# Optimization experiments

Hardware: AMD Instinct MI355X
Metric: run time of the kernel (lower is better)

Reference implementation:

```python
import jax, jax.numpy as jnp
import numpy as np

N_NODES = 50000
N_EDGES = 800000
OUT_DIM = 394
BN_EPS = 1e-5


def setup_inputs() -> dict:
    key = jax.random.key(0)
    ks = jax.random.split(key, 10)
    x = jax.random.normal(ks[0], (N_NODES, 2), dtype=jnp.float32)
    edge_index = jax.random.randint(ks[1], (2, N_EDGES), 0, N_NODES, dtype=jnp.int64)
    W_gcn = jax.random.normal(ks[2], (OUT_DIM, 2), dtype=jnp.float32) * 0.5
    b_gcn = jax.random.normal(ks[3], (OUT_DIM,), dtype=jnp.float32) * 0.1
    bn_gamma = jax.random.normal(ks[4], (OUT_DIM,), dtype=jnp.float32) * 0.1 + 1.0
    bn_beta = jax.random.normal(ks[5], (OUT_DIM,), dtype=jnp.float32) * 0.1
    bn_mean = jax.random.normal(ks[6], (OUT_DIM,), dtype=jnp.float32) * 0.1
    bn_var = jax.random.uniform(ks[7], (OUT_DIM,), dtype=jnp.float32, minval=0.5, maxval=1.5)
    fc_w = jax.random.normal(ks[8], (OUT_DIM, OUT_DIM), dtype=jnp.float32) * (1.0 / np.sqrt(OUT_DIM))
    fc_b = jax.random.normal(ks[9], (OUT_DIM,), dtype=jnp.float32) * 0.1
    return {"x": x, "edge_index": edge_index, "W_gcn": W_gcn, "b_gcn": b_gcn,
            "bn_gamma": bn_gamma, "bn_beta": bn_beta, "bn_mean": bn_mean,
            "bn_var": bn_var, "fc_w": fc_w, "fc_b": fc_b}


def reference(x, edge_index, W_gcn, b_gcn, bn_gamma, bn_beta, bn_mean, bn_var, fc_w, fc_b):
    n = x.shape[0]
    loop = jnp.arange(n, dtype=edge_index.dtype)
    # PyG GCNConv: add self-loops, symmetric deg^{-1/2} normalization
    src = jnp.concatenate([edge_index[0], loop])  # [E+N] message sources
    dst = jnp.concatenate([edge_index[1], loop])  # [E+N] message targets
    deg = jax.ops.segment_sum(jnp.ones_like(dst, dtype=x.dtype), dst, num_segments=n)
    dinv = jnp.where(deg > 0, jax.lax.rsqrt(deg), 0.0)
    norm = dinv[src] * dinv[dst]  # [E+N]
    xl = x @ W_gcn.T  # [N, 394] linear transform before aggregation
    msgs = xl[src] * norm[:, None]  # [E+N, 394] gathered + normalized messages
    agg = jax.ops.segment_sum(msgs, dst, num_segments=n) + b_gcn  # scatter-add
    h = jax.nn.relu(agg)
    # BatchNorm1d in eval mode (running stats)
    h = (h - bn_mean) * jax.lax.rsqrt(bn_var + BN_EPS) * bn_gamma + bn_beta
    # dropout is a no-op in eval mode
    z = h @ fc_w.T + fc_b
    return (jax.nn.log_softmax(z, axis=1), z)
```

## Files before the change

kernel.cpp:

```cpp
#include <hip/hip_runtime.h>
#include <math.h>

#define DIM 394
#define KP  416
#define NT  13
#define NP  448
#define BN_EPS 1e-5f
#define MAXD 96

typedef __bf16 bf16x8 __attribute__((ext_vector_type(8)));
typedef float  f32x4  __attribute__((ext_vector_type(4)));

__device__ inline bool edges_are_int32(const int* ei) {
    int l = threadIdx.x & 63;
    unsigned long long b = __ballot(ei[2 * l + 1] != 0);
    return b != 0ULL;
}


__global__ void prep_kernel(const float* __restrict__ Wg, const float* __restrict__ bg,
                            const float* __restrict__ gamma, const float* __restrict__ beta,
                            const float* __restrict__ mean, const float* __restrict__ var,
                            const float* __restrict__ fcw,
                            uint4* __restrict__ zbase, float4* __restrict__ Pk,
                            float* __restrict__ Ok, bf16x8* __restrict__ Bp,
                            int z4, int zb) {
    int b = blockIdx.x, t = threadIdx.x;
    if (b < zb) {
        int i = b * 256 + t;
        if (i < z4) zbase[i] = make_uint4(0u, 0u, 0u, 0u);
    } else if (b < zb + 2) {
        int k = (b - zb) * 256 + t;
        if (k < KP) {
            float4 p = make_float4(0.f, 0.f, 0.f, 0.f);
            float o = 0.f;
            if (k < DIM) {
                p.x = Wg[2 * k];
                p.y = Wg[2 * k + 1];
                p.z = bg[k];
                float s = gamma[k] * rsqrtf(var[k] + BN_EPS);
                p.w = s;
                o = beta[k] - s * mean[k];
            }
            Pk[k] = p;
            Ok[k] = o;
        }
    } else {
        int idx = (b - zb - 2) * 256 + t;
        if (idx < NT * 4 * NP) {
            int col = idx % NP;
            int r   = idx / NP;
            int k0  = r * 8;
            bf16x8 v;
            #pragma unroll
            for (int q = 0; q < 8; ++q) {
                int k = k0 + q;
                float f = (col < DIM && k < DIM) ? fcw[col * DIM + k] : 0.0f;
                v[q] = (__bf16)f;
            }
            Bp[idx] = v;
        }
    }
}

__global__ void place_kernel(const int* __restrict__ ei,
                             unsigned* __restrict__ degc,
                             unsigned* __restrict__ payload,
                             unsigned* __restrict__ ocnt,
                             uint2* __restrict__ olist, int e) {
    bool is32 = edges_are_int32(ei);
    int i0 = (blockIdx.x * blockDim.x + threadIdx.x) * 4;
    if (i0 >= e) return;
    int s[4], d[4];
    int cnt = 4;
    if (i0 + 4 <= e) {
        if (is32) {
            int4 sv = *reinterpret_cast<const int4*>(&ei[i0]);
            int4 dv = *reinterpret_cast<const int4*>(&ei[e + i0]);
            s[0] = sv.x; s[1] = sv.y; s[2] = sv.z; s[3] = sv.w;
            d[0] = dv.x; d[1] = dv.y; d[2] = dv.z; d[3] = dv.w;
        } else {
            int4 a = *reinterpret_cast<const int4*>(&ei[2 * i0]);
            int4 b = *reinterpret_cast<const int4*>(&ei[2 * i0 + 4]);
            int4 c = *reinterpret_cast<const int4*>(&ei[2 * (e + i0)]);
            int4 dd = *reinterpret_cast<const int4*>(&ei[2 * (e + i0) + 4]);
            s[0] = a.x; s[1] = a.z; s[2] = b.x; s[3] = b.z;
            d[0] = c.x; d[1] = c.z; d[2] = dd.x; d[3] = dd.z;
        }
    } else {
        cnt = e - i0;
        for (int j = 0; j < cnt; ++j) {
            s[j] = is32 ? ei[i0 + j]     : ei[2 * (i0 + j)];
            d[j] = is32 ? ei[e + i0 + j] : ei[2 * (e + i0 + j)];
        }
    }
    #pragma unroll
    for (int j = 0; j < 4; ++j) {
        if (j >= cnt) break;
        unsigned t = atomicAdd(&degc[d[j]], 1u);
        if (t < MAXD) {
            payload[(size_t)d[j] * MAXD + t] = (unsigned)s[j];
        } else {
            unsigned o = atomicAdd(ocnt, 1u);
            olist[o] = make_uint2((unsigned)s[j], (unsigned)d[j]);
        }
    }
}

__global__ void cleanup_kernel(const uint2* __restrict__ olist,
                               const unsigned* __restrict__ ocnt,
                               const unsigned* __restrict__ degc,
                               const float2* __restrict__ x2,
                               float* __restrict__ yover) {
    unsigned cnt = *ocnt;
    int gstride = gridDim.x * blockDim.x;
    for (unsigned i = blockIdx.x * blockDim.x + threadIdx.x; i < cnt; i += gstride) {
        uint2 sd = olist[i];
        float ds = rsqrtf(1.0f + (float)degc[sd.x]);
        float2 xv = x2[sd.x];
        atomicAdd(&yover[2 * sd.y],     ds * xv.x);
        atomicAdd(&yover[2 * sd.y + 1], ds * xv.y);
    }
}

__global__ __launch_bounds__(256, 2)
void gemm_fused(const float2* __restrict__ x2, const unsigned* __restrict__ degc,
                const unsigned* __restrict__ payload, const float* __restrict__ yover,
                const float4* __restrict__ Pk, const float* __restrict__ Ok,
                const bf16x8* __restrict__ Bp, const float* __restrict__ fcb,
                float* __restrict__ outp, float* __restrict__ z, int n) {
    __shared__ bf16x8 As[2][256];
    __shared__ float2 red[64][4];

    int tid = threadIdx.x;
    int wv  = tid >> 6;
    int l   = tid & 63;
    int cg_ = tid & 15;
    int kg  = l >> 4;
    int row0 = blockIdx.x * 64;
    int gi = row0 + l;

    float y0 = 0.f, y1 = 0.f;
    {
        float2 psum = make_float2(0.f, 0.f);
        float dinv_i = 0.f;
        float2 xi = make_float2(0.f, 0.f);
        if (gi < n) {
            unsigned dg = degc[gi];
            dinv_i = rsqrtf(1.0f + (float)dg);
            xi = x2[gi];
            unsigned m = dg < MAXD ? dg : MAXD;
            const unsigned* pl = payload + (size_t)gi * MAXD;
            for (unsigned t = wv; t < m; t += 4) {
                unsigned s = pl[t];
                float2 xv = x2[s];
                float ds = rsqrtf(1.0f + (float)degc[s]);
                psum.x = fmaf(ds, xv.x, psum.x);
                psum.y = fmaf(ds, xv.y, psum.y);
            }
            if (wv == 0) {
                psum.x += yover[2 * gi];
                psum.y += yover[2 * gi + 1];
            }
        }
        red[l][wv] = psum;
        __syncthreads();
        if (gi < n) {
            float sx = red[l][0].x + red[l][1].x + red[l][2].x + red[l][3].x;
            float sy = red[l][0].y + red[l][1].y + red[l][2].y + red[l][3].y;
            y0 = dinv_i * (sx + dinv_i * xi.x);
            y1 = dinv_i * (sy + dinv_i * xi.y);
        }
    }

    f32x4 acc[4][7];
    #pragma unroll
    for (int a = 0; a < 4; ++a)
        #pragma unroll
        for (int b = 0; b < 7; ++b)
            acc[a][b] = (f32x4){0.f, 0.f, 0.f, 0.f};

    auto stageA = [&](int ks, int buf) {
        int kb = ks * 32 + wv * 8;
        bf16x8 hv;
        #pragma unroll
        for (int q = 0; q < 8; ++q) {
            float4 p = Pk[kb + q];
            float t = fmaf(y0, p.x, fmaf(y1, p.y, p.z));
            t = fmaxf(t, 0.f);
            hv[q] = (__bf16)fmaf(p.w, t, Ok[kb + q]);
        }
        As[buf][wv * 64 + l] = hv;
    };

    const bf16x8* bptr = Bp + (kg * 448 + wv * 112 + cg_);

    bf16x8 Bcur[7], Bnxt[7];
    #pragma unroll
    for (int c = 0; c < 7; ++c) Bcur[c] = bptr[c * 16];
    stageA(0, 0);
    __syncthreads();

    int buf = 0;
    for (int ks = 0; ks < NT; ++ks) {
        if (ks < NT - 1) {
            const bf16x8* bn = bptr + (size_t)(ks + 1) * (4 * 448);
            #pragma unroll
            for (int c = 0; c < 7; ++c) Bnxt[c] = bn[c * 16];
            stageA(ks + 1, buf ^ 1);
        }
        bf16x8 af[4];
        #pragma unroll
        for (int rt = 0; rt < 4; ++rt)
            af[rt] = As[buf][kg * 64 + rt * 16 + cg_];
        #pragma unroll
        for (int ct = 0; ct < 7; ++ct)
            #pragma unroll
            for (int rt = 0; rt < 4; ++rt)
                acc[rt][ct] = __builtin_amdgcn_mfma_f32_16x16x32_bf16(
                                  af[rt], Bcur[ct], acc[rt][ct], 0, 0, 0);
        __syncthreads();
        #pragma unroll
        for (int c = 0; c < 7; ++c) Bcur[c] = Bnxt[c];
        buf ^= 1;
    }

    float* redm = (float*)&As[0][0];
    float* reds = redm + 256;

    int colb = wv * 112;
    float bias[7];
    bool  cv[7];
    #pragma unroll
    for (int ct = 0; ct < 7; ++ct) {
        int c = colb + ct * 16 + cg_;
        cv[ct] = (c < DIM);
        bias[ct] = cv[ct] ? fcb[c] : 0.f;
    }
    #pragma unroll
    for (int rt = 0; rt < 4; ++rt)
        #pragma unroll
        for (int ct = 0; ct < 7; ++ct)
            acc[rt][ct] = acc[rt][ct] + bias[ct];

    f32x4 mx[4];
    #pragma unroll
    for (int rt = 0; rt < 4; ++rt) {
        f32x4 m = (f32x4){-1e30f, -1e30f, -1e30f, -1e30f};
        #pragma unroll
        for (int ct = 0; ct < 7; ++ct) {
            if (!cv[ct]) continue;
            #pragma unroll
            for (int j = 0; j < 4; ++j) m[j] = fmaxf(m[j], acc[rt][ct][j]);
        }
        #pragma unroll
        for (int msk = 1; msk < 16; msk <<= 1)
            #pragma unroll
            for (int j = 0; j < 4; ++j)
                m[j] = fmaxf(m[j], __shfl_xor(m[j], msk));
        mx[rt] = m;
    }
    if (cg_ == 0) {
        #pragma unroll
        for (int rt = 0; rt < 4; ++rt)
            #pragma unroll
            for (int j = 0; j < 4; ++j)
                redm[(rt * 16 + kg * 4 + j) * 4 + wv] = mx[rt][j];
    }
    __syncthreads();
    f32x4 gm[4];
    #pragma unroll
    for (int rt = 0; rt < 4; ++rt)
        #pragma unroll
        for (int j = 0; j < 4; ++j) {
            int r = (rt * 16 + kg * 4 + j) * 4;
            gm[rt][j] = fmaxf(fmaxf(redm[r], redm[r + 1]),
                              fmaxf(redm[r + 2], redm[r + 3]));
        }

    f32x4 sm[4];
    #pragma unroll
    for (int rt = 0; rt < 4; ++rt) {
        f32x4 s = (f32x4){0.f, 0.f, 0.f, 0.f};
        #pragma unroll
        for (int ct = 0; ct < 7; ++ct) {
            if (!cv[ct]) continue;
            #pragma unroll
            for (int j = 0; j < 4; ++j)
                s[j] += __expf(acc[rt][ct][j] - gm[rt][j]);
        }
        #pragma unroll
        for (int msk = 1; msk < 16; msk <<= 1)
            #pragma unroll
            for (int j = 0; j < 4; ++j)
                s[j] += __shfl_xor(s[j], msk);
        sm[rt] = s;
    }
    if (cg_ == 0) {
        #pragma unroll
        for (int rt = 0; rt < 4; ++rt)
            #pragma unroll
            for (int j = 0; j < 4; ++j)
                reds[(rt * 16 + kg * 4 + j) * 4 + wv] = sm[rt][j];
    }
    __syncthreads();
    f32x4 lse[4];
    #pragma unroll
    for (int rt = 0; rt < 4; ++rt)
        #pragma unroll
        for (int j = 0; j < 4; ++j) {
            int r = (rt * 16 + kg * 4 + j) * 4;
            float t = reds[r] + reds[r + 1] + reds[r + 2] + reds[r + 3];
            lse[rt][j] = gm[rt][j] + __logf(t);
        }

    #pragma unroll
    for (int rt = 0; rt < 4; ++rt)
        #pragma unroll
        for (int j = 0; j < 4; ++j) {
            int grow = row0 + rt * 16 + kg * 4 + j;
            if (grow >= n) continue;
            size_t base = (size_t)grow * DIM;
            float L = lse[rt][j];
            #pragma unroll
            for (int ct = 0; ct < 7; ++ct) {
                if (!cv[ct]) continue;
                int c = colb + ct * 16 + cg_;
                float zv = acc[rt][ct][j];
                z[base + c]    = zv;
                outp[base + c] = zv - L;
            }
        }
}

extern "C" void kernel_launch(void* const* d_in, const int* in_sizes, int n_in,
                              void* d_out, int out_size, void* d_ws, size_t ws_size,
                              hipStream_t stream) {
    int n = in_sizes[0] / 2;
    int e = in_sizes[1] / 2;

    const float2* x2   = (const float2*)d_in[0];
    const int*   ei    = (const int*)d_in[1];
    const float* Wg    = (const float*)d_in[2];
    const float* bg    = (const float*)d_in[3];
    const float* gamma = (const float*)d_in[4];
    const float* beta  = (const float*)d_in[5];
    const float* mean  = (const float*)d_in[6];
    const float* var   = (const float*)d_in[7];
    const float* fcw   = (const float*)d_in[8];
    const float* fcb   = (const float*)d_in[9];

    float* out = (float*)d_out;
    float* z   = out + (size_t)n * DIM;

    char* wsb = (char*)d_ws;
    unsigned* degc  = (unsigned*)wsb;
    float*    yover = (float*)(degc + n);
    unsigned* ocnt  = (unsigned*)(yover + 2 * (size_t)n);
    uint2*    olist = (uint2*)(ocnt + 4);
    unsigned* payload = (unsigned*)(olist + e);
    size_t off = (size_t)(3 * n + 4) * 4 + (size_t)e * 8 + (size_t)n * MAXD * 4;
    off = (off + 255) & ~(size_t)255;
    bf16x8* Bp = (bf16x8*)(wsb + off);
    off += (size_t)NT * 4 * NP * 16;
    float4* Pk = (float4*)(wsb + off);
    off += (size_t)KP * 16;
    float* Ok  = (float*)(wsb + off);

    int zwords = 3 * n + 4;
    int z4 = (zwords + 3) / 4;
    int zb = (z4 + 255) / 256;
    int prep_blocks = zb + 2 + (NT * 4 * NP + 255) / 256;
    int eb4 = (e / 4 + 255) / 256 + 1;

    prep_kernel<<<prep_blocks, 256, 0, stream>>>(Wg, bg, gamma, beta, mean, var,
                                                 fcw, (uint4*)degc, Pk, Ok, Bp,
                                                 z4, zb);
    place_kernel<<<eb4, 256, 0, stream>>>(ei, degc, payload, ocnt, olist, e);
    cleanup_kernel<<<64, 256, 0, stream>>>(olist, ocnt, degc, x2, yover);

    int gm = (n + 63) / 64;
    gemm_fused<<<gm, 256, 0, stream>>>(x2, degc, payload, yover, Pk, Ok, Bp,
                                       fcb, out, z, n);
}
```

Before: 129.0 us.

## Split neighbor gather into its own kernel and halve GEMM row tile

```diff
diff --git a/kernel.cpp b/kernel.cpp
--- a/kernel.cpp
+++ b/kernel.cpp
@@ -6,9 +6,10 @@
 #define NT  13
 #define NP  448
 #define BN_EPS 1e-5f
-#define MAXD 96
+#define MAXD 32
 
 typedef __bf16 bf16x8 __attribute__((ext_vector_type(8)));
+typedef __bf16 bf16x4 __attribute__((ext_vector_type(4)));
 typedef float  f32x4  __attribute__((ext_vector_type(4)));
 
 __device__ inline bool edges_are_int32(const int* ei) {
@@ -123,74 +124,79 @@
     }
 }
 
-__global__ __launch_bounds__(256, 2)
-void gemm_fused(const float2* __restrict__ x2, const unsigned* __restrict__ degc,
-                const unsigned* __restrict__ payload, const float* __restrict__ yover,
+__global__ __launch_bounds__(256)
+void gather_kernel(const float2* __restrict__ x2, const unsigned* __restrict__ degc,
+                   const unsigned* __restrict__ payload, const float* __restrict__ yover,
+                   float2* __restrict__ y2, int n) {
+    int tid = blockIdx.x * blockDim.x + threadIdx.x;
+    int gi = tid >> 2;
+    int ln = tid & 3;
+    if (gi >= n) return;
+    unsigned dg = degc[gi];
+    unsigned m = dg < MAXD ? dg : MAXD;
+    const unsigned* pl = payload + (size_t)gi * MAXD;
+    float sx = 0.f, sy = 0.f;
+    for (unsigned t = ln; t < m; t += 4) {
+        unsigned s = pl[t];
+        float ds = rsqrtf(1.0f + (float)degc[s]);
+        float2 xv = x2[s];
+        sx = fmaf(ds, xv.x, sx);
+        sy = fmaf(ds, xv.y, sy);
+    }
+    sx += __shfl_xor(sx, 1); sy += __shfl_xor(sy, 1);
+    sx += __shfl_xor(sx, 2); sy += __shfl_xor(sy, 2);
+    if (ln == 0) {
+        float di = rsqrtf(1.0f + (float)dg);
+        float2 xi = x2[gi];
+        sx += yover[2 * gi];
+        sy += yover[2 * gi + 1];
+        y2[gi] = make_float2(di * (sx + di * xi.x), di * (sy + di * xi.y));
+    }
+}
+
+__global__ __launch_bounds__(256, 3)
+void gemm_fused(const float2* __restrict__ y2,
                 const float4* __restrict__ Pk, const float* __restrict__ Ok,
                 const bf16x8* __restrict__ Bp, const float* __restrict__ fcb,
                 float* __restrict__ outp, float* __restrict__ z, int n) {
-    __shared__ bf16x8 As[2][256];
-    __shared__ float2 red[64][4];
+    __shared__ bf16x4 As4[2][256];
 
     int tid = threadIdx.x;
     int wv  = tid >> 6;
     int l   = tid & 63;
     int cg_ = tid & 15;
     int kg  = l >> 4;
-    int row0 = blockIdx.x * 64;
-    int gi = row0 + l;
-
+    int row0 = blockIdx.x * 32;
+
+    int srow = tid & 31;
+    int skc  = (tid >> 5) & 3;
+    int shalf = tid >> 7;
+    int gi = row0 + srow;
     float y0 = 0.f, y1 = 0.f;
-    {
-        float2 psum = make_float2(0.f, 0.f);
-        float dinv_i = 0.f;
-        float2 xi = make_float2(0.f, 0.f);
-        if (gi < n) {
-            unsigned dg = degc[gi];
-            dinv_i = rsqrtf(1.0f + (float)dg);
-            xi = x2[gi];
-            unsigned m = dg < MAXD ? dg : MAXD;
-            const unsigned* pl = payload + (size_t)gi * MAXD;
-            for (unsigned t = wv; t < m; t += 4) {
-                unsigned s = pl[t];
-                float2 xv = x2[s];
-                float ds = rsqrtf(1.0f + (float)degc[s]);
-                psum.x = fmaf(ds, xv.x, psum.x);
-                psum.y = fmaf(ds, xv.y, psum.y);
-            }
-            if (wv == 0) {
-                psum.x += yover[2 * gi];
-                psum.y += yover[2 * gi + 1];
-            }
-        }
-        red[l][wv] = psum;
-        __syncthreads();
-        if (gi < n) {
-            float sx = red[l][0].x + red[l][1].x + red[l][2].x + red[l][3].x;
-            float sy = red[l][0].y + red[l][1].y + red[l][2].y + red[l][3].y;
-            y0 = dinv_i * (sx + dinv_i * xi.x);
-            y1 = dinv_i * (sy + dinv_i * xi.y);
-        }
-    }
-
-    f32x4 acc[4][7];
-    #pragma unroll
-    for (int a = 0; a < 4; ++a)
+    if (gi < n) {
+        float2 yv = y2[gi];
+        y0 = yv.x;
+        y1 = yv.y;
+    }
+
+    f32x4 acc[2][7];
+    #pragma unroll
+    for (int a = 0; a < 2; ++a)
         #pragma unroll
         for (int b = 0; b < 7; ++b)
             acc[a][b] = (f32x4){0.f, 0.f, 0.f, 0.f};
 
     auto stageA = [&](int ks, int buf) {
-        int kb = ks * 32 + wv * 8;
-        bf16x8 hv;
-        #pragma unroll
-        for (int q = 0; q < 8; ++q) {
+        int kb = ks * 32 + skc * 8 + shalf * 4;
+        bf16x4 hv;
+        #pragma unroll
+        for (int q = 0; q < 4; ++q) {
             float4 p = Pk[kb + q];
             float t = fmaf(y0, p.x, fmaf(y1, p.y, p.z));
             t = fmaxf(t, 0.f);
             hv[q] = (__bf16)fmaf(p.w, t, Ok[kb + q]);
         }
-        As[buf][wv * 64 + l] = hv;
+        As4[buf][(skc * 32 + srow) * 2 + shalf] = hv;
     };
 
     const bf16x8* bptr = Bp + (kg * 448 + wv * 112 + cg_);
@@ -209,14 +215,15 @@
             for (int c = 0; c < 7; ++c) Bnxt[c] = bn[c * 16];
             stageA(ks + 1, buf ^ 1);
         }
-        bf16x8 af[4];
-        #pragma unroll
-        for (int rt = 0; rt < 4; ++rt)
-            af[rt] = As[buf][kg * 64 + rt * 16 + cg_];
+        const bf16x8* As8 = (const bf16x8*)&As4[buf][0];
+        bf16x8 af[2];
+        #pragma unroll
+        for (int rt = 0; rt < 2; ++rt)
+            af[rt] = As8[kg * 32 + rt * 16 + cg_];
         #pragma unroll
         for (int ct = 0; ct < 7; ++ct)
             #pragma unroll
-            for (int rt = 0; rt < 4; ++rt)
+            for (int rt = 0; rt < 2; ++rt)
                 acc[rt][ct] = __builtin_amdgcn_mfma_f32_16x16x32_bf16(
                                   af[rt], Bcur[ct], acc[rt][ct], 0, 0, 0);
         __syncthreads();
@@ -225,8 +232,8 @@
         buf ^= 1;
     }
 
-    float* redm = (float*)&As[0][0];
-    float* reds = redm + 256;
+    float* redm = (float*)&As4[0][0];
+    float* reds = redm + 128;
 
     int colb = wv * 112;
     float bias[7];
@@ -238,14 +245,14 @@
         bias[ct] = cv[ct] ? fcb[c] : 0.f;
     }
     #pragma unroll
-    for (int rt = 0; rt < 4; ++rt)
+    for (int rt = 0; rt < 2; ++rt)
         #pragma unroll
         for (int ct = 0; ct < 7; ++ct)
             acc[rt][ct] = acc[rt][ct] + bias[ct];
 
-    f32x4 mx[4];
-    #pragma unroll
-    for (int rt = 0; rt < 4; ++rt) {
+    f32x4 mx[2];
+    #pragma unroll
+    for (int rt = 0; rt < 2; ++rt) {
         f32x4 m = (f32x4){-1e30f, -1e30f, -1e30f, -1e30f};
         #pragma unroll
         for (int ct = 0; ct < 7; ++ct) {
@@ -262,15 +269,15 @@
     }
     if (cg_ == 0) {
         #pragma unroll
-        for (int rt = 0; rt < 4; ++rt)
+        for (int rt = 0; rt < 2; ++rt)
             #pragma unroll
             for (int j = 0; j < 4; ++j)
                 redm[(rt * 16 + kg * 4 + j) * 4 + wv] = mx[rt][j];
     }
     __syncthreads();
-    f32x4 gm[4];
-    #pragma unroll
-    for (int rt = 0; rt < 4; ++rt)
+    f32x4 gm[2];
+    #pragma unroll
+    for (int rt = 0; rt < 2; ++rt)
         #pragma unroll
         for (int j = 0; j < 4; ++j) {
             int r = (rt * 16 + kg * 4 + j) * 4;
@@ -278,9 +285,9 @@
                               fmaxf(redm[r + 2], redm[r + 3]));
         }
 
-    f32x4 sm[4];
-    #pragma unroll
-    for (int rt = 0; rt < 4; ++rt) {
+    f32x4 sm[2];
+    #pragma unroll
+    for (int rt = 0; rt < 2; ++rt) {
         f32x4 s = (f32x4){0.f, 0.f, 0.f, 0.f};
         #pragma unroll
         for (int ct = 0; ct < 7; ++ct) {
@@ -298,15 +305,15 @@
     }
     if (cg_ == 0) {
         #pragma unroll
-        for (int rt = 0; rt < 4; ++rt)
+        for (int rt = 0; rt < 2; ++rt)
             #pragma unroll
             for (int j = 0; j < 4; ++j)
                 reds[(rt * 16 + kg * 4 + j) * 4 + wv] = sm[rt][j];
     }
     __syncthreads();
-    f32x4 lse[4];
-    #pragma unroll
-    for (int rt = 0; rt < 4; ++rt)
+    f32x4 lse[2];
+    #pragma unroll
+    for (int rt = 0; rt < 2; ++rt)
         #pragma unroll
         for (int j = 0; j < 4; ++j) {
             int r = (rt * 16 + kg * 4 + j) * 4;
@@ -315,7 +322,7 @@
         }
 
     #pragma unroll
-    for (int rt = 0; rt < 4; ++rt)
+    for (int rt = 0; rt < 2; ++rt)
         #pragma unroll
         for (int j = 0; j < 4; ++j) {
             int grow = row0 + rt * 16 + kg * 4 + j;
@@ -357,9 +364,12 @@
     unsigned* degc  = (unsigned*)wsb;
     float*    yover = (float*)(degc + n);
     unsigned* ocnt  = (unsigned*)(yover + 2 * (size_t)n);
-    uint2*    olist = (uint2*)(ocnt + 4);
-    unsigned* payload = (unsigned*)(olist + e);
-    size_t off = (size_t)(3 * n + 4) * 4 + (size_t)e * 8 + (size_t)n * MAXD * 4;
+    float2*   y2    = (float2*)(ocnt + 4);
+    uint2*    olist = (uint2*)(y2 + n);
+    size_t off = (size_t)(5 * n + 4) * 4 + (size_t)e * 8;
+    off = (off + 255) & ~(size_t)255;
+    unsigned* payload = (unsigned*)(wsb + off);
+    off += (size_t)n * MAXD * 4;
     off = (off + 255) & ~(size_t)255;
     bf16x8* Bp = (bf16x8*)(wsb + off);
     off += (size_t)NT * 4 * NP * 16;
@@ -378,8 +388,9 @@
                                                  z4, zb);
     place_kernel<<<eb4, 256, 0, stream>>>(ei, degc, payload, ocnt, olist, e);
     cleanup_kernel<<<64, 256, 0, stream>>>(olist, ocnt, degc, x2, yover);
-
-    int gm = (n + 63) / 64;
-    gemm_fused<<<gm, 256, 0, stream>>>(x2, degc, payload, yover, Pk, Ok, Bp,
-                                       fcb, out, z, n);
-}
+    gather_kernel<<<(4 * n + 255) / 256, 256, 0, stream>>>(x2, degc, payload,
+                                                           yover, y2, n);
+
+    int gm = (n + 31) / 32;
+    gemm_fused<<<gm, 256, 0, stream>>>(y2, Pk, Ok, Bp, fcb, out, z, n);
+}
```

Result: slower. 143.4 us (+11.2%).

## Fuse edge placement with weight packing and fold overflow edges into GEMM kernel

Applied to the files above, without the earlier changes.

```diff
diff --git a/kernel.cpp b/kernel.cpp
--- a/kernel.cpp
+++ b/kernel.cpp
@@ -6,7 +6,7 @@
 #define NT  13
 #define NP  448
 #define BN_EPS 1e-5f
-#define MAXD 96
+#define MAXD 32
 
 typedef __bf16 bf16x8 __attribute__((ext_vector_type(8)));
 typedef float  f32x4  __attribute__((ext_vector_type(4)));
@@ -18,19 +18,61 @@
 }
 
 
-__global__ void prep_kernel(const float* __restrict__ Wg, const float* __restrict__ bg,
-                            const float* __restrict__ gamma, const float* __restrict__ beta,
-                            const float* __restrict__ mean, const float* __restrict__ var,
-                            const float* __restrict__ fcw,
-                            uint4* __restrict__ zbase, float4* __restrict__ Pk,
-                            float* __restrict__ Ok, bf16x8* __restrict__ Bp,
-                            int z4, int zb) {
+__global__ void place_pack_kernel(const int* __restrict__ ei,
+                                  unsigned* __restrict__ degc,
+                                  unsigned* __restrict__ payload,
+                                  unsigned* __restrict__ ocnt,
+                                  uint2* __restrict__ olist, int e, int eb4,
+                                  const float* __restrict__ Wg,
+                                  const float* __restrict__ bg,
+                                  const float* __restrict__ gamma,
+                                  const float* __restrict__ beta,
+                                  const float* __restrict__ mean,
+                                  const float* __restrict__ var,
+                                  const float* __restrict__ fcw,
+                                  float4* __restrict__ Pk, float* __restrict__ Ok,
+                                  bf16x8* __restrict__ Bp) {
     int b = blockIdx.x, t = threadIdx.x;
-    if (b < zb) {
-        int i = b * 256 + t;
-        if (i < z4) zbase[i] = make_uint4(0u, 0u, 0u, 0u);
-    } else if (b < zb + 2) {
-        int k = (b - zb) * 256 + t;
+    if (b < eb4) {
+        bool is32 = edges_are_int32(ei);
+        int i0 = (b * 256 + t) * 4;
+        if (i0 >= e) return;
+        int s[4], d[4];
+        int cnt = 4;
+        if (i0 + 4 <= e) {
+            if (is32) {
+                int4 sv = *reinterpret_cast<const int4*>(&ei[i0]);
+                int4 dv = *reinterpret_cast<const int4*>(&ei[e + i0]);
+                s[0] = sv.x; s[1] = sv.y; s[2] = sv.z; s[3] = sv.w;
+                d[0] = dv.x; d[1] = dv.y; d[2] = dv.z; d[3] = dv.w;
+            } else {
+                int4 a = *reinterpret_cast<const int4*>(&ei[2 * i0]);
+                int4 bb = *reinterpret_cast<const int4*>(&ei[2 * i0 + 4]);
+                int4 c = *reinterpret_cast<const int4*>(&ei[2 * (e + i0)]);
+                int4 dd = *reinterpret_cast<const int4*>(&ei[2 * (e + i0) + 4]);
+                s[0] = a.x; s[1] = a.z; s[2] = bb.x; s[3] = bb.z;
+                d[0] = c.x; d[1] = c.z; d[2] = dd.x; d[3] = dd.z;
+            }
+        } else {
+            cnt = e - i0;
+            for (int j = 0; j < cnt; ++j) {
+                s[j] = is32 ? ei[i0 + j]     : ei[2 * (i0 + j)];
+                d[j] = is32 ? ei[e + i0 + j] : ei[2 * (e + i0 + j)];
+            }
+        }
+        #pragma unroll
+        for (int j = 0; j < 4; ++j) {
+            if (j >= cnt) break;
+            unsigned tk = atomicAdd(&degc[d[j]], 1u);
+            if (tk < MAXD) {
+                payload[(size_t)d[j] * MAXD + tk] = (unsigned)s[j];
+            } else {
+                unsigned o = atomicAdd(ocnt, 1u);
+                olist[o] = make_uint2((unsigned)s[j], (unsigned)d[j]);
+            }
+        }
+    } else if (b < eb4 + 2) {
+        int k = (b - eb4) * 256 + t;
         if (k < KP) {
             float4 p = make_float4(0.f, 0.f, 0.f, 0.f);
             float o = 0.f;
@@ -38,15 +80,15 @@
                 p.x = Wg[2 * k];
                 p.y = Wg[2 * k + 1];
                 p.z = bg[k];
-                float s = gamma[k] * rsqrtf(var[k] + BN_EPS);
-                p.w = s;
-                o = beta[k] - s * mean[k];
+                float sc = gamma[k] * rsqrtf(var[k] + BN_EPS);
+                p.w = sc;
+                o = beta[k] - sc * mean[k];
             }
             Pk[k] = p;
             Ok[k] = o;
         }
     } else {
-        int idx = (b - zb - 2) * 256 + t;
+        int idx = (b - eb4 - 2) * 256 + t;
         if (idx < NT * 4 * NP) {
             int col = idx % NP;
             int r   = idx / NP;
@@ -63,69 +105,10 @@
     }
 }
 
-__global__ void place_kernel(const int* __restrict__ ei,
-                             unsigned* __restrict__ degc,
-                             unsigned* __restrict__ payload,
-                             unsigned* __restrict__ ocnt,
-                             uint2* __restrict__ olist, int e) {
-    bool is32 = edges_are_int32(ei);
-    int i0 = (blockIdx.x * blockDim.x + threadIdx.x) * 4;
-    if (i0 >= e) return;
-    int s[4], d[4];
-    int cnt = 4;
-    if (i0 + 4 <= e) {
-        if (is32) {
-            int4 sv = *reinterpret_cast<const int4*>(&ei[i0]);
-            int4 dv = *reinterpret_cast<const int4*>(&ei[e + i0]);
-            s[0] = sv.x; s[1] = sv.y; s[2] = sv.z; s[3] = sv.w;
-            d[0] = dv.x; d[1] = dv.y; d[2] = dv.z; d[3] = dv.w;
-        } else {
-            int4 a = *reinterpret_cast<const int4*>(&ei[2 * i0]);
-            int4 b = *reinterpret_cast<const int4*>(&ei[2 * i0 + 4]);
-            int4 c = *reinterpret_cast<const int4*>(&ei[2 * (e + i0)]);
-            int4 dd = *reinterpret_cast<const int4*>(&ei[2 * (e + i0) + 4]);
-            s[0] = a.x; s[1] = a.z; s[2] = b.x; s[3] = b.z;
-            d[0] = c.x; d[1] = c.z; d[2] = dd.x; d[3] = dd.z;
-        }
-    } else {
-        cnt = e - i0;
-        for (int j = 0; j < cnt; ++j) {
-            s[j] = is32 ? ei[i0 + j]     : ei[2 * (i0 + j)];
-            d[j] = is32 ? ei[e + i0 + j] : ei[2 * (e + i0 + j)];
-        }
-    }
-    #pragma unroll
-    for (int j = 0; j < 4; ++j) {
-        if (j >= cnt) break;
-        unsigned t = atomicAdd(&degc[d[j]], 1u);
-        if (t < MAXD) {
-            payload[(size_t)d[j] * MAXD + t] = (unsigned)s[j];
-        } else {
-            unsigned o = atomicAdd(ocnt, 1u);
-            olist[o] = make_uint2((unsigned)s[j], (unsigned)d[j]);
-        }
-    }
-}
-
-__global__ void cleanup_kernel(const uint2* __restrict__ olist,
-                               const unsigned* __restrict__ ocnt,
-                               const unsigned* __restrict__ degc,
-                               const float2* __restrict__ x2,
-                               float* __restrict__ yover) {
-    unsigned cnt = *ocnt;
-    int gstride = gridDim.x * blockDim.x;
-    for (unsigned i = blockIdx.x * blockDim.x + threadIdx.x; i < cnt; i += gstride) {
-        uint2 sd = olist[i];
-        float ds = rsqrtf(1.0f + (float)degc[sd.x]);
-        float2 xv = x2[sd.x];
-        atomicAdd(&yover[2 * sd.y],     ds * xv.x);
-        atomicAdd(&yover[2 * sd.y + 1], ds * xv.y);
-    }
-}
-
 __global__ __launch_bounds__(256, 2)
 void gemm_fused(const float2* __restrict__ x2, const unsigned* __restrict__ degc,
-                const unsigned* __restrict__ payload, const float* __restrict__ yover,
+                const unsigned* __restrict__ payload,
+                const unsigned* __restrict__ ocnt, const uint2* __restrict__ olist,
                 const float4* __restrict__ Pk, const float* __restrict__ Ok,
                 const bf16x8* __restrict__ Bp, const float* __restrict__ fcb,
                 float* __restrict__ outp, float* __restrict__ z, int n) {
@@ -159,8 +142,16 @@
                 psum.y = fmaf(ds, xv.y, psum.y);
             }
             if (wv == 0) {
-                psum.x += yover[2 * gi];
-                psum.y += yover[2 * gi + 1];
+                unsigned cnt = *ocnt;
+                for (unsigned j = 0; j < cnt; ++j) {
+                    uint2 sd = olist[j];
+                    if ((int)sd.y == gi) {
+                        float2 xv = x2[sd.x];
+                        float ds = rsqrtf(1.0f + (float)degc[sd.x]);
+                        psum.x = fmaf(ds, xv.x, psum.x);
+                        psum.y = fmaf(ds, xv.y, psum.y);
+                    }
+                }
             }
         }
         red[l][wv] = psum;
@@ -355,11 +346,12 @@
 
     char* wsb = (char*)d_ws;
     unsigned* degc  = (unsigned*)wsb;
-    float*    yover = (float*)(degc + n);
-    unsigned* ocnt  = (unsigned*)(yover + 2 * (size_t)n);
+    unsigned* ocnt  = (unsigned*)(degc + n);
     uint2*    olist = (uint2*)(ocnt + 4);
-    unsigned* payload = (unsigned*)(olist + e);
-    size_t off = (size_t)(3 * n + 4) * 4 + (size_t)e * 8 + (size_t)n * MAXD * 4;
+    size_t off = (size_t)(n + 4) * 4 + (size_t)e * 8;
+    off = (off + 255) & ~(size_t)255;
+    unsigned* payload = (unsigned*)(wsb + off);
+    off += (size_t)n * MAXD * 4;
     off = (off + 255) & ~(size_t)255;
     bf16x8* Bp = (bf16x8*)(wsb + off);
     off += (size_t)NT * 4 * NP * 16;
@@ -367,19 +359,15 @@
     off += (size_t)KP * 16;
     float* Ok  = (float*)(wsb + off);
 
-    int zwords = 3 * n + 4;
-    int z4 = (zwords + 3) / 4;
-    int zb = (z4 + 255) / 256;
-    int prep_blocks = zb + 2 + (NT * 4 * NP + 255) / 256;
+    hipMemsetAsync(degc, 0, (size_t)(n + 4) * 4, stream);
+
     int eb4 = (e / 4 + 255) / 256 + 1;
-
-    prep_kernel<<<prep_blocks, 256, 0, stream>>>(Wg, bg, gamma, beta, mean, var,
-                                                 fcw, (uint4*)degc, Pk, Ok, Bp,
-                                                 z4, zb);
-    place_kernel<<<eb4, 256, 0, stream>>>(ei, degc, payload, ocnt, olist, e);
-    cleanup_kernel<<<64, 256, 0, stream>>>(olist, ocnt, degc, x2, yover);
+    int pack_blocks = 2 + (NT * 4 * NP + 255) / 256;
+    place_pack_kernel<<<eb4 + pack_blocks, 256, 0, stream>>>(
+        ei, degc, payload, ocnt, olist, e, eb4,
+        Wg, bg, gamma, beta, mean, var, fcw, Pk, Ok, Bp);
 
     int gm = (n + 63) / 64;
-    gemm_fused<<<gm, 256, 0, stream>>>(x2, degc, payload, yover, Pk, Ok, Bp,
-                                       fcb, out, z, n);
+    gemm_fused<<<gm, 256, 0, stream>>>(x2, degc, payload, ocnt, olist,
+                                       Pk, Ok, Bp, fcb, out, z, n);
 }
```

Measured after the change: 139.9 us. +8.4%, slower.
